# Kernel tuning notes

Hardware: AMD Instinct MI355X
Metric: run time of the kernel (lower is better)

## Reference

```python
import jax, jax.numpy as jnp
import numpy as np

MARGIN = 0.5
BETA = 0.0
K = 5

def setup_inputs() -> dict:
    key = jax.random.key(0)
    k1, k2 = jax.random.split(key)
    n, d, n_classes = 4096, 512, 512
    inputs = jax.random.normal(k1, (n, d), dtype=jnp.float32)
    # L2-normalize as is standard for similarity-based DML embeddings
    inputs = inputs / jnp.linalg.norm(inputs, axis=1, keepdims=True)
    targets = jax.random.randint(k2, (n,), 0, n_classes, dtype=jnp.int64)
    return {"inputs": inputs, "targets": targets}

def reference(inputs, targets):
    n = inputs.shape[0]
    sim = inputs @ inputs.T                      # [n, n] similarity matrix
    same = targets[:, None] == targets[None, :]  # [n, n] same-class mask
    eye = jnp.eye(n, dtype=bool)
    pos_mask = same & ~eye                       # positive pairs (off-diagonal)
    neg_mask = ~same                             # negative pairs
    # margin_loss (hinge on similarity): pos -> [margin + beta - s]_+, neg -> [margin + s - beta]_+
    pos_l = jnp.maximum(MARGIN + BETA - sim, 0.0)
    neg_l = jnp.maximum(MARGIN + sim - BETA, 0.0)
    valid = pos_mask | neg_mask
    pair_loss = jnp.where(pos_mask, pos_l, neg_l)  # per-pair loss where valid
    num_of_zeros = jnp.sum(valid & (pair_loss == 0.0))
    # top-(4K) over the multiset of all valid pair losses (== topk of concat(pos_loss, neg_loss))
    masked = jnp.where(valid, pair_loss, -jnp.inf).reshape(-1)
    top_loss, _ = jax.lax.top_k(masked, 4 * K)
    loss = jnp.mean(top_loss)
    mean_pos_sim = jnp.sum(jnp.where(pos_mask, sim, 0.0)) / jnp.sum(pos_mask)
    mean_neg_sim = jnp.sum(jnp.where(neg_mask, sim, 0.0)) / jnp.sum(neg_mask)
    # NOTE: the original swaps the names: it returns mean(pos_sim) as `mean_neg_sim` and vice versa.
    return (loss, num_of_zeros, mean_pos_sim, mean_neg_sim)
```

## Files before the change

### kernel.cpp

```cpp
#include <hip/hip_runtime.h>
#include <hip/hip_fp16.h>

constexpr int N = 4096;
constexpr int D = 512;
constexpr int NT = 32;
constexpr int NBLK = NT * (NT + 1) / 2;
constexpr int BCAP = 256;
constexpr float CAND_TH = 0.62f;

typedef _Float16 f16x8 __attribute__((ext_vector_type(8)));
typedef float f32x4 __attribute__((ext_vector_type(4)));

__device__ __forceinline__ void load_lds16(const _Float16* g, _Float16* l) {
  __builtin_amdgcn_global_load_lds(
      (const __attribute__((address_space(1))) void*)g,
      (__attribute__((address_space(3))) void*)l, 16, 0, 0);
}

__global__ void prep_kernel(const float4* __restrict__ X4,
                            ushort4* __restrict__ Xh4) {
  int gid = blockIdx.x * 256 + threadIdx.x;
  float4 v = X4[gid];
  ushort4 o;
  o.x = __half_as_ushort(__float2half_rn(v.x));
  o.y = __half_as_ushort(__float2half_rn(v.y));
  o.z = __half_as_ushort(__float2half_rn(v.z));
  o.w = __half_as_ushort(__float2half_rn(v.w));
  Xh4[gid] = o;
}

__global__ __launch_bounds__(256, 4) void gemm_stats_kernel(
    const _Float16* __restrict__ Xh, const int* __restrict__ tgt,
    float* __restrict__ slots, float* __restrict__ cand) {
  float* blk_sumv = slots;
  float* blk_sump = slots + NBLK;
  unsigned* blk_cntv = (unsigned*)(slots + 2 * NBLK);
  unsigned* blk_cntp = (unsigned*)(slots + 3 * NBLK);
  unsigned* blk_zero = (unsigned*)(slots + 4 * NBLK);
  unsigned* blk_ccnt = (unsigned*)(slots + 5 * NBLK);

  __shared__ _Float16 As[128 * 64];
  __shared__ _Float16 Bs[128 * 64];
  __shared__ int tA[128], tB[128];
  __shared__ float redf[2][4];
  __shared__ unsigned redu[3][4];
  __shared__ float bc_buf[BCAP];
  __shared__ unsigned bc_cnt;

  int tid = threadIdx.x;
  if (tid == 0) bc_cnt = 0;

  int id = blockIdx.x, br = 0;
  while (id >= (NT - br)) { id -= (NT - br); br++; }
  int bc = br + id;

  if (tid < 128) tA[tid] = tgt[br * 128 + tid];
  else           tB[tid - 128] = tgt[bc * 128 + (tid - 128)];

  int lane = tid & 63, wave = tid >> 6;
  int wm = (wave >> 1) << 6;
  int wn = (wave & 1) << 6;
  int lrow = lane & 15;
  int q4 = lane >> 4;
  int x7 = lrow & 7;
  int quad4 = q4 * 4;

  int srow[4], scol[4], sdst[4];
#pragma unroll
  for (int i = 0; i < 4; i++) {
    int C = (i * 4 + wave) * 64 + lane;
    int row = C >> 3, p = C & 7;
    srow[i] = row;
    scol[i] = (p ^ (row & 7)) * 8;
    sdst[i] = (i * 4 + wave) * 512;
  }
  const _Float16* Arow = Xh + (size_t)(br * 128) * D;
  const _Float16* Brow = Xh + (size_t)(bc * 128) * D;

  f32x4 acc[4][4] = {};

  for (int k0 = 0; k0 < D; k0 += 64) {
    __syncthreads();
#pragma unroll
    for (int i = 0; i < 4; i++) {
      load_lds16(Arow + srow[i] * D + k0 + scol[i], As + sdst[i]);
      load_lds16(Brow + srow[i] * D + k0 + scol[i], Bs + sdst[i]);
    }
    __syncthreads();
#pragma unroll
    for (int ks = 0; ks < 64; ks += 32) {
      int c0 = ks >> 3;
      f16x8 af[4], bf[4];
#pragma unroll
      for (int mi = 0; mi < 4; mi++)
        af[mi] = *(const f16x8*)&As[(wm + mi * 16 + lrow) * 64 +
                                    ((c0 + q4) ^ x7) * 8];
#pragma unroll
      for (int ni = 0; ni < 4; ni++)
        bf[ni] = *(const f16x8*)&Bs[(wn + ni * 16 + lrow) * 64 +
                                    ((c0 + q4) ^ x7) * 8];
#pragma unroll
      for (int mi = 0; mi < 4; mi++)
#pragma unroll
        for (int ni = 0; ni < 4; ni++)
          acc[mi][ni] = __builtin_amdgcn_mfma_f32_16x16x32_f16(
              af[mi], bf[ni], acc[mi][ni], 0, 0, 0);
    }
  }

  int ti[4][4], tj[4];
#pragma unroll
  for (int ni = 0; ni < 4; ni++) tj[ni] = tB[wn + ni * 16 + lrow];
#pragma unroll
  for (int mi = 0; mi < 4; mi++)
#pragma unroll
    for (int r = 0; r < 4; r++) ti[mi][r] = tA[wm + mi * 16 + quad4 + r];

  float lsv = 0.f, lsp = 0.f;
  unsigned lcv = 0, lcp = 0, lz = 0;
  int ibase = br * 128 + wm + quad4;
  int jbase = bc * 128 + wn + lrow;

#pragma unroll
  for (int mi = 0; mi < 4; mi++)
#pragma unroll
    for (int ni = 0; ni < 4; ni++)
#pragma unroll
      for (int r = 0; r < 4; r++) {
        float s = acc[mi][ni][r];
        int i = ibase + mi * 16 + r;
        int j = jbase + ni * 16;
        bool valid = j > i;
        bool pos = valid && (ti[mi][r] == tj[ni]);
        float t = pos ? -s : s;
        float loss = fmaxf(0.5f + t, 0.0f);
        if (valid) { lsv += s; lcv++; if (loss == 0.0f) lz++; }
        if (pos) { lsp += s; lcp++; }
        if (valid && (loss > CAND_TH)) {
          unsigned p = atomicAdd(&bc_cnt, 1u);
          if (p < BCAP) bc_buf[p] = loss;
        }
      }

#pragma unroll
  for (int o = 32; o > 0; o >>= 1) {
    lsv += __shfl_down(lsv, o);
    lsp += __shfl_down(lsp, o);
    lcv += __shfl_down(lcv, o);
    lcp += __shfl_down(lcp, o);
    lz  += __shfl_down(lz, o);
  }
  if (lane == 0) {
    redf[0][wave] = lsv; redf[1][wave] = lsp;
    redu[0][wave] = lcv; redu[1][wave] = lcp; redu[2][wave] = lz;
  }
  __syncthreads();
  unsigned n = bc_cnt < BCAP ? bc_cnt : BCAP;
  if (tid == 0) {
    int b = blockIdx.x;
    blk_sumv[b] = redf[0][0] + redf[0][1] + redf[0][2] + redf[0][3];
    blk_sump[b] = redf[1][0] + redf[1][1] + redf[1][2] + redf[1][3];
    blk_cntv[b] = redu[0][0] + redu[0][1] + redu[0][2] + redu[0][3];
    blk_cntp[b] = redu[1][0] + redu[1][1] + redu[1][2] + redu[1][3];
    blk_zero[b] = redu[2][0] + redu[2][1] + redu[2][2] + redu[2][3];
    blk_ccnt[b] = n;
  }
  for (unsigned i2 = tid; i2 < n; i2 += 256)
    cand[blockIdx.x * BCAP + i2] = bc_buf[i2];
}

__device__ __forceinline__ void ins10(float (&t)[10], float v) {
#pragma unroll
  for (int k = 9; k > 0; k--) t[k] = fmaxf(t[k], fminf(v, t[k - 1]));
  t[0] = fmaxf(t[0], v);
}

__global__ void finalize_kernel(const float* __restrict__ slots,
                                const float* __restrict__ cand,
                                float* __restrict__ out) {
  const float* blk_sumv = slots;
  const float* blk_sump = slots + NBLK;
  const unsigned* blk_cntv = (const unsigned*)(slots + 2 * NBLK);
  const unsigned* blk_cntp = (const unsigned*)(slots + 3 * NBLK);
  const unsigned* blk_zero = (const unsigned*)(slots + 4 * NBLK);
  const unsigned* blk_ccnt = (const unsigned*)(slots + 5 * NBLK);

  __shared__ float Lf[256 * 10];
  __shared__ float rf[2][4];
  __shared__ unsigned ru[3][4];

  int tid = threadIdx.x;
  int lane = tid & 63, wave = tid >> 6;

  float sv = 0.f, sp = 0.f;
  unsigned cv = 0, cp = 0, zz = 0;
  for (int b = tid; b < NBLK; b += 256) {
    sv += blk_sumv[b]; sp += blk_sump[b];
    cv += blk_cntv[b]; cp += blk_cntp[b]; zz += blk_zero[b];
  }
#pragma unroll
  for (int o = 32; o > 0; o >>= 1) {
    sv += __shfl_down(sv, o);
    sp += __shfl_down(sp, o);
    cv += __shfl_down(cv, o);
    cp += __shfl_down(cp, o);
    zz += __shfl_down(zz, o);
  }
  if (lane == 0) {
    rf[0][wave] = sv; rf[1][wave] = sp;
    ru[0][wave] = cv; ru[1][wave] = cp; ru[2][wave] = zz;
  }

  float t[10];
#pragma unroll
  for (int k = 0; k < 10; k++) t[k] = -1e30f;
  for (int b = tid; b < NBLK; b += 256) {
    unsigned n = blk_ccnt[b];
    for (unsigned i = 0; i < n; i++) ins10(t, cand[b * BCAP + i]);
  }
#pragma unroll
  for (int k = 0; k < 10; k++) Lf[tid * 10 + k] = t[k];

  for (int s = 128; s >= 1; s >>= 1) {
    __syncthreads();
    if (tid < s) {
#pragma unroll
      for (int k = 0; k < 10; k++) ins10(t, Lf[(tid + s) * 10 + k]);
#pragma unroll
      for (int k = 0; k < 10; k++) Lf[tid * 10 + k] = t[k];
    }
  }
  __syncthreads();

  if (tid == 0) {
    float topsum = 0.f;
#pragma unroll
    for (int k = 0; k < 10; k++) topsum += t[k];
    float tsv = rf[0][0] + rf[0][1] + rf[0][2] + rf[0][3];
    float tsp = rf[1][0] + rf[1][1] + rf[1][2] + rf[1][3];
    unsigned tcv = ru[0][0] + ru[0][1] + ru[0][2] + ru[0][3];
    unsigned tcp = ru[1][0] + ru[1][1] + ru[1][2] + ru[1][3];
    unsigned tzz = ru[2][0] + ru[2][1] + ru[2][2] + ru[2][3];
    out[0] = topsum * 0.1f;
    out[1] = (float)(2u * tzz);
    out[2] = tsp / (float)tcp;
    out[3] = (tsv - tsp) / (float)(tcv - tcp);
  }
}

extern "C" void kernel_launch(void* const* d_in, const int* in_sizes, int n_in,
                              void* d_out, int out_size, void* d_ws, size_t ws_size,
                              hipStream_t stream) {
  const float* X = (const float*)d_in[0];
  const int* tgt = (const int*)d_in[1];
  float* out = (float*)d_out;
  char* ws = (char*)d_ws;

  float* slots = (float*)ws;
  float* cand = (float*)(ws + 12672);
  _Float16* Xh = (_Float16*)(ws + 12672 + 540672);

  prep_kernel<<<(N * D / 4) / 256, 256, 0, stream>>>((const float4*)X,
                                                     (ushort4*)Xh);
  gemm_stats_kernel<<<NBLK, 256, 0, stream>>>(Xh, tgt, slots, cand);
  finalize_kernel<<<1, 256, 0, stream>>>(slots, cand, out);
}
```

Before: 118.2 us.

## Double-buffer GEMM LDS tiles, wave-aggregate candidate atomics, parallelize finalize scan

The GEMM main loop now double-buffers A/B tiles in LDS, issuing the next k-slab's global-to-LDS loads before computing on the current one. Raw s_waitcnt/s_barrier calls replace the paired __syncthreads, so load latency can overlap MFMA work. Candidate insertion uses a wave ballot with a single atomic per wave instead of one LDS atomic per element. Finalize stages the per-block counts in LDS and spreads each block's candidates across threads rather than giving each thread whole blocks. The trade-off is doubled LDS usage and launch bounds lowered to 2 blocks per CU, which reduces occupancy.

```diff
diff --git a/kernel.cpp b/kernel.cpp
--- a/kernel.cpp
+++ b/kernel.cpp
@@ -11,11 +11,18 @@
 typedef _Float16 f16x8 __attribute__((ext_vector_type(8)));
 typedef float f32x4 __attribute__((ext_vector_type(4)));
 
+#define BAR() asm volatile("s_barrier" ::: "memory")
+#define WAITV8() asm volatile("s_waitcnt vmcnt(8)" ::: "memory")
+#define WAITV0() asm volatile("s_waitcnt vmcnt(0)" ::: "memory")
+
 __device__ __forceinline__ void load_lds16(const _Float16* g, _Float16* l) {
   __builtin_amdgcn_global_load_lds(
       (const __attribute__((address_space(1))) void*)g,
       (__attribute__((address_space(3))) void*)l, 16, 0, 0);
 }
+
+constexpr int CAND_OFF = 12672;
+constexpr int XH_OFF = 553344;
 
 __global__ void prep_kernel(const float4* __restrict__ X4,
                             ushort4* __restrict__ Xh4) {
@@ -29,7 +36,7 @@
   Xh4[gid] = o;
 }
 
-__global__ __launch_bounds__(256, 4) void gemm_stats_kernel(
+__global__ __launch_bounds__(256, 2) void gemm_stats_kernel(
     const _Float16* __restrict__ Xh, const int* __restrict__ tgt,
     float* __restrict__ slots, float* __restrict__ cand) {
   float* blk_sumv = slots;
@@ -39,8 +46,8 @@
   unsigned* blk_zero = (unsigned*)(slots + 4 * NBLK);
   unsigned* blk_ccnt = (unsigned*)(slots + 5 * NBLK);
 
-  __shared__ _Float16 As[128 * 64];
-  __shared__ _Float16 Bs[128 * 64];
+  __shared__ _Float16 As[2 * 128 * 64];
+  __shared__ _Float16 Bs[2 * 128 * 64];
   __shared__ int tA[128], tB[128];
   __shared__ float redf[2][4];
   __shared__ unsigned redu[3][4];
@@ -77,27 +84,41 @@
   const _Float16* Arow = Xh + (size_t)(br * 128) * D;
   const _Float16* Brow = Xh + (size_t)(bc * 128) * D;
 
+  auto issue = [&](int k0, int sel) {
+#pragma unroll
+    for (int i = 0; i < 4; i++) {
+      load_lds16(Arow + srow[i] * D + k0 + scol[i], As + sel * 8192 + sdst[i]);
+      load_lds16(Brow + srow[i] * D + k0 + scol[i], Bs + sel * 8192 + sdst[i]);
+    }
+  };
+
   f32x4 acc[4][4] = {};
 
-  for (int k0 = 0; k0 < D; k0 += 64) {
-    __syncthreads();
-#pragma unroll
-    for (int i = 0; i < 4; i++) {
-      load_lds16(Arow + srow[i] * D + k0 + scol[i], As + sdst[i]);
-      load_lds16(Brow + srow[i] * D + k0 + scol[i], Bs + sdst[i]);
-    }
-    __syncthreads();
+  __syncthreads();
+  issue(0, 0);
+
+#pragma unroll
+  for (int it = 0; it < 8; ++it) {
+    int sel = it & 1;
+    if (it > 0) BAR();
+    if (it < 7) {
+      issue((it + 1) * 64, sel ^ 1);
+      WAITV8();
+    } else {
+      WAITV0();
+    }
+    BAR();
 #pragma unroll
     for (int ks = 0; ks < 64; ks += 32) {
       int c0 = ks >> 3;
       f16x8 af[4], bf[4];
 #pragma unroll
       for (int mi = 0; mi < 4; mi++)
-        af[mi] = *(const f16x8*)&As[(wm + mi * 16 + lrow) * 64 +
+        af[mi] = *(const f16x8*)&As[sel * 8192 + (wm + mi * 16 + lrow) * 64 +
                                     ((c0 + q4) ^ x7) * 8];
 #pragma unroll
       for (int ni = 0; ni < 4; ni++)
-        bf[ni] = *(const f16x8*)&Bs[(wn + ni * 16 + lrow) * 64 +
+        bf[ni] = *(const f16x8*)&Bs[sel * 8192 + (wn + ni * 16 + lrow) * 64 +
                                     ((c0 + q4) ^ x7) * 8];
 #pragma unroll
       for (int mi = 0; mi < 4; mi++)
@@ -136,9 +157,16 @@
         float loss = fmaxf(0.5f + t, 0.0f);
         if (valid) { lsv += s; lcv++; if (loss == 0.0f) lz++; }
         if (pos) { lsp += s; lcp++; }
-        if (valid && (loss > CAND_TH)) {
-          unsigned p = atomicAdd(&bc_cnt, 1u);
-          if (p < BCAP) bc_buf[p] = loss;
+        bool cp = valid && (loss > CAND_TH);
+        unsigned long long m = __ballot(cp);
+        if (m) {
+          unsigned wb = 0;
+          if (lane == 0) wb = atomicAdd(&bc_cnt, (unsigned)__popcll(m));
+          wb = (unsigned)__shfl((int)wb, 0);
+          if (cp) {
+            unsigned pos2 = wb + (unsigned)__popcll(m & ((1ull << lane) - 1));
+            if (pos2 < BCAP) bc_buf[pos2] = loss;
+          }
         }
       }
 
@@ -185,6 +213,7 @@
   const unsigned* blk_zero = (const unsigned*)(slots + 4 * NBLK);
   const unsigned* blk_ccnt = (const unsigned*)(slots + 5 * NBLK);
 
+  __shared__ unsigned cnts[NBLK];
   __shared__ float Lf[256 * 10];
   __shared__ float rf[2][4];
   __shared__ unsigned ru[3][4];
@@ -197,6 +226,7 @@
   for (int b = tid; b < NBLK; b += 256) {
     sv += blk_sumv[b]; sp += blk_sump[b];
     cv += blk_cntv[b]; cp += blk_cntp[b]; zz += blk_zero[b];
+    cnts[b] = blk_ccnt[b];
   }
 #pragma unroll
   for (int o = 32; o > 0; o >>= 1) {
@@ -210,13 +240,14 @@
     rf[0][wave] = sv; rf[1][wave] = sp;
     ru[0][wave] = cv; ru[1][wave] = cp; ru[2][wave] = zz;
   }
+  __syncthreads();
 
   float t[10];
 #pragma unroll
   for (int k = 0; k < 10; k++) t[k] = -1e30f;
-  for (int b = tid; b < NBLK; b += 256) {
-    unsigned n = blk_ccnt[b];
-    for (unsigned i = 0; i < n; i++) ins10(t, cand[b * BCAP + i]);
+  for (int b = 0; b < NBLK; b++) {
+    unsigned n = cnts[b];
+    for (unsigned i = tid; i < n; i += 256) ins10(t, cand[b * BCAP + i]);
   }
 #pragma unroll
   for (int k = 0; k < 10; k++) Lf[tid * 10 + k] = t[k];
@@ -257,8 +288,8 @@
   char* ws = (char*)d_ws;
 
   float* slots = (float*)ws;
-  float* cand = (float*)(ws + 12672);
-  _Float16* Xh = (_Float16*)(ws + 12672 + 540672);
+  float* cand = (float*)(ws + CAND_OFF);
+  _Float16* Xh = (_Float16*)(ws + XH_OFF);
 
   prep_kernel<<<(N * D / 4) / 256, 256, 0, stream>>>((const float4*)X,
                                                      (ushort4*)Xh);
```

Result: slower. 271.1 us (+129.4%).
